# Performance work log

Measured on AMD Instinct MI355X. Metric: run time of the kernel, lower is better.

## Reference

```python
import jax, jax.numpy as jnp
import numpy as np

RES = (160, 160, 160)            # (X, Y, Z)
AABB_MIN, AABB_MAX = -1.3, 1.3
DEG = 2
SH_DIM = (DEG + 1) ** 2          # 9
N_SAMPLES = 480                  # 'plenoxels': mean(res)*3*voxel_mul
NEAR, FAR = 0.2, 6.0
WHITE_BKGD = True
N_RAYS = 2048

C0 = 0.28209479177387814
C1 = 0.4886025119029199
C2 = (1.0925484305920792, -1.0925484305920792, 0.31539156525252005,
      -1.0925484305920792, 0.5462742152960396)


def sh_encoder(dirs):
    # real spherical harmonics up to degree 2 of the normalized view dir
    d = dirs / jnp.linalg.norm(dirs, axis=-1, keepdims=True)
    x, y, z = d[..., 0], d[..., 1], d[..., 2]
    return jnp.stack([
        jnp.full_like(x, C0),
        -C1 * y, C1 * z, -C1 * x,
        C2[0] * x * y, C2[1] * y * z,
        C2[2] * (2.0 * z * z - x * x - y * y),
        C2[3] * x * z, C2[4] * (x * x - y * y),
    ], axis=-1)                                     # [..., 9]


def trilinear_sample(grid, coords):
    # grid: [C, X, Y, Z]; coords: [..., 3] in (-1, 1).
    # torch F.grid_sample convention: coord x indexes last dim (Z), y -> Y, z -> X.
    # align_corners=True, padding_mode='zeros'.
    Cc, X, Y, Z = grid.shape
    gf = grid.reshape(Cc, -1)
    fx = (coords[..., 0] + 1.0) * 0.5 * (Z - 1)
    fy = (coords[..., 1] + 1.0) * 0.5 * (Y - 1)
    fz = (coords[..., 2] + 1.0) * 0.5 * (X - 1)
    x0f = jnp.floor(fx); y0f = jnp.floor(fy); z0f = jnp.floor(fz)
    wx = fx - x0f; wy = fy - y0f; wz = fz - z0f
    x0 = x0f.astype(jnp.int32); y0 = y0f.astype(jnp.int32); z0 = z0f.astype(jnp.int32)
    out = jnp.zeros(coords.shape[:-1] + (Cc,), dtype=grid.dtype)
    for dz in (0, 1):
        for dy in (0, 1):
            for dx in (0, 1):
                ix = x0 + dx; iy = y0 + dy; iz = z0 + dz
                valid = ((ix >= 0) & (ix < Z) & (iy >= 0) & (iy < Y)
                         & (iz >= 0) & (iz < X))
                w = ((wx if dx else 1.0 - wx)
                     * (wy if dy else 1.0 - wy)
                     * (wz if dz else 1.0 - wz)) * valid
                lin = (jnp.clip(iz, 0, X - 1) * Y + jnp.clip(iy, 0, Y - 1)) * Z \
                      + jnp.clip(ix, 0, Z - 1)
                vals = jnp.take(gf, lin, axis=1)    # [C, ...]
                out = out + jnp.moveaxis(vals, 0, -1) * w[..., None]
    return out                                      # [..., C]


def get_intersections(rays_o, rays_d, aabb, step, n):
    off_pos = (aabb[1] - rays_o) / rays_d
    off_neg = (aabb[0] - rays_o) / rays_d
    start = jnp.max(jnp.minimum(off_pos, off_neg), axis=-1, keepdims=True)
    start = jnp.clip(start, NEAR, FAR)
    steps = jnp.arange(n, dtype=rays_o.dtype)[None, :]
    return start + steps * step                     # [N, n]


def setup_inputs() -> dict:
    key = jax.random.key(0)
    k1, k2, k3, k4 = jax.random.split(key, 4)
    rays_o = jax.random.normal(k1, (N_RAYS, 3), jnp.float32) * 0.1   # inside aabb
    rays_d = jax.random.normal(k2, (N_RAYS, 3), jnp.float32)
    sigma_data = 0.1 + 0.05 * jax.random.normal(k3, (1,) + RES, jnp.float32)
    rgb_data = 0.01 * jax.random.normal(k4, (3 * SH_DIM,) + RES, jnp.float32)
    return {"rays_o": rays_o, "rays_d": rays_d,
            "sigma_data": sigma_data, "rgb_data": rgb_data}


def reference(rays_o, rays_d, sigma_data, rgb_data):
    dt = rays_o.dtype
    aabb = jnp.array([[AABB_MIN] * 3, [AABB_MAX] * 3], dtype=dt)
    aabb_size = aabb[1] - aabb[0]
    inv_aabb_size = 2.0 / aabb_size
    step = jnp.linalg.norm(aabb_size) / N_SAMPLES   # voxel_len

    inter = jax.lax.stop_gradient(
        get_intersections(rays_o, rays_d, aabb, step, N_SAMPLES))  # [N,S]
    pts = rays_o[:, None, :] + rays_d[:, None, :] * inter[:, :-1, None]  # [N,S-1,3]
    pn = (pts - aabb[0]) * inv_aabb_size - 1.0       # normalized (-1,1)

    sigma = jax.nn.relu(trilinear_sample(sigma_data, pn)[..., 0])   # [N,S-1]

    dists = jnp.diff(inter, axis=1) * jnp.linalg.norm(rays_d, axis=-1, keepdims=True)
    alpha = 1.0 - jnp.exp(-sigma * dists)
    cum_light = jnp.concatenate(
        [jnp.ones((alpha.shape[0], 1), dtype=dt),
         jnp.cumprod(1.0 - alpha[:, :-1] + 1e-10, axis=-1)], axis=-1)
    abs_light = alpha * cum_light                    # [N,S-1]

    sh_mult = sh_encoder(rays_d)                     # [N,9]
    rgb_feat = trilinear_sample(rgb_data, pn)        # [N,S-1,27]
    rgb_feat = rgb_feat.reshape(rgb_feat.shape[0], rgb_feat.shape[1], 3, SH_DIM)
    sh_rgb = jnp.einsum('nsck,nk->nsc', rgb_feat, sh_mult)

    rgb = jax.nn.sigmoid(sh_rgb)
    rgb_map = jnp.einsum('ns,nsc->nc', abs_light, rgb)
    if WHITE_BKGD:
        rgb_map = rgb_map + (1.0 - abs_light.sum(-1, keepdims=True))
    return rgb_map
```

## Files before the change

### kernel.cpp

```cpp
#include <hip/hip_runtime.h>
#include <math.h>

#define RESN  160
#define VOX   4096000
#define YSTR  160
#define ZSTR  25600
#define NPTS  478
#define NRAYS 2048
#define REC   32

typedef float f2_u __attribute__((ext_vector_type(2), aligned(4)));

__global__ __launch_bounds__(256)
void transpose_grid(const float* __restrict__ sig, const float* __restrict__ rgb,
                    unsigned short* __restrict__ rec)
{
    const int v = blockIdx.x * 256 + threadIdx.x;
    float vals[32];
    vals[0] = sig[v];
    #pragma unroll
    for (int k = 0; k < 27; ++k) vals[1 + k] = rgb[(size_t)k * VOX + v];
    vals[28] = vals[29] = vals[30] = vals[31] = 0.f;
    unsigned short h[32];
    #pragma unroll
    for (int k = 0; k < 32; ++k) {
        unsigned u = __float_as_uint(vals[k]);
        unsigned r = (u + 0x7FFFu + ((u >> 16) & 1u)) >> 16;
        h[k] = (unsigned short)r;
    }
    uint4* dst = (uint4*)(rec + (size_t)v * REC);
    const uint4* src = (const uint4*)h;
    #pragma unroll
    for (int i = 0; i < 4; ++i) dst[i] = src[i];
}

__device__ __forceinline__ void bf2(unsigned u, float& lo, float& hi) {
    lo = __uint_as_float(u << 16);
    hi = __uint_as_float(u & 0xFFFF0000u);
}

__global__ __launch_bounds__(256)
void plenoxel_render2(const float* __restrict__ rays_o,
                      const float* __restrict__ rays_d,
                      const unsigned short* __restrict__ rec,
                      float* __restrict__ out)
{
    const int ray  = blockIdx.x;
    const int tid  = threadIdx.x;
    const int wave = tid >> 6;
    const int lane = tid & 63;

    const float ox = rays_o[ray*3+0], oy = rays_o[ray*3+1], oz = rays_o[ray*3+2];
    const float dxr = rays_d[ray*3+0], dyr = rays_d[ray*3+1], dzr = rays_d[ray*3+2];

    const float h = 2.6f * 1.7320508075688772f / 480.0f;

    const float ax = (1.3f - ox) / dxr, bx = (-1.3f - ox) / dxr;
    const float ay = (1.3f - oy) / dyr, by = (-1.3f - oy) / dyr;
    const float az = (1.3f - oz) / dzr, bz = (-1.3f - oz) / dzr;
    float start = fmaxf(fmaxf(fminf(ax, bx), fminf(ay, by)), fminf(az, bz));
    start = fminf(fmaxf(start, 0.2f), 6.0f);

    const float B = 1.3164f;
    const float mx1 = ( B - ox) / dxr, mx0 = (-B - ox) / dxr;
    const float my1 = ( B - oy) / dyr, my0 = (-B - oy) / dyr;
    const float mz1 = ( B - oz) / dzr, mz0 = (-B - oz) / dzr;
    float tl = fmaxf(fmaxf(fminf(mx0, mx1), fminf(my0, my1)), fminf(mz0, mz1));
    float th = fminf(fminf(fmaxf(mx0, mx1), fmaxf(my0, my1)), fmaxf(mz0, mz1));
    tl = fmaxf(tl, start);
    th = fminf(th, fmaf((float)NPTS, h, start));
    int s_lo, s_hi;
    if (th < tl) { s_lo = 0; s_hi = -1; }
    else {
        s_lo = max(0,    (int)floorf((tl - start) / h) - 1);
        s_hi = min(NPTS, (int)ceilf ((th - start) / h) + 1);
    }

    const float dsq  = dxr*dxr + dyr*dyr + dzr*dzr;
    const float dinv = rsqrtf(dsq);
    const float dn   = sqrtf(dsq);
    const float X = dxr * dinv, Y = dyr * dinv, Z = dzr * dinv;
    const float shv[9] = {
        0.28209479177387814f,
        -0.4886025119029199f * Y,
         0.4886025119029199f * Z,
        -0.4886025119029199f * X,
         1.0925484305920792f * X * Y,
        -1.0925484305920792f * Y * Z,
         0.31539156525252005f * (2.0f * Z * Z - X * X - Y * Y),
        -1.0925484305920792f * X * Z,
         0.5462742152960396f * (X * X - Y * Y),
    };
    const float dist = h * dn;

    float accR = 0.f, accG = 0.f, accB = 0.f, accL = 0.f;
    float carry = 1.0f;

    const int nlive = s_hi - s_lo + 1;
    if (nlive > 0) {
        const int chunk = (nlive + 3) >> 2;
        const int my_lo = s_lo + wave * chunk;
        const int my_hi = min(my_lo + chunk - 1, s_hi);

        for (int basei = my_lo; basei <= my_hi; basei += 64) {
            const int s = basei + lane;
            float alpha = 0.f, cr = 0.f, cg = 0.f, cb = 0.f;
            if (s <= my_hi) {
                const float t  = fmaf((float)s, h, start);
                const float px = fmaf(dxr, t, ox);
                const float py = fmaf(dyr, t, oy);
                const float pz = fmaf(dzr, t, oz);
                const float fx = fmaf(px, 61.153846153846f, 79.5f);
                const float fy = fmaf(py, 61.153846153846f, 79.5f);
                const float fz = fmaf(pz, 61.153846153846f, 79.5f);
                const float fxf = floorf(fx), fyf = floorf(fy), fzf = floorf(fz);
                const int   x0 = (int)fxf, y0 = (int)fyf, z0 = (int)fzf;
                const float wx1 = fx - fxf, wy1 = fy - fyf, wz1 = fz - fzf;
                const float wx0 = 1.f - wx1, wy0 = 1.f - wy1, wz0 = 1.f - wz1;

                float sv = 0.f, a0 = 0.f, a1 = 0.f, a2 = 0.f;

                if (x0 >= 0 && x0 <= 158 && y0 >= 0 && y0 <= 158 && z0 >= 0 && z0 <= 158) {
                    const float wzy[4] = { wz0*wy0, wz0*wy1, wz1*wy0, wz1*wy1 };
                    const int   offp[4] = { 0, YSTR*REC, ZSTR*REC, (ZSTR+YSTR)*REC };
                    const size_t base = ((size_t)z0 * ZSTR + (size_t)y0 * YSTR + x0) * REC;
                    #pragma unroll
                    for (int p = 0; p < 4; ++p) {
                        const uint4* P = (const uint4*)(rec + base + offp[p]);
                        uint4 q0[4], q1[4];
                        q0[0]=P[0]; q0[1]=P[1]; q0[2]=P[2]; q0[3]=P[3];
                        q1[0]=P[4]; q1[1]=P[5]; q1[2]=P[6]; q1[3]=P[7];
                        const float wA = wzy[p] * wx0, wB = wzy[p] * wx1;
                        #pragma unroll
                        for (int q = 0; q < 4; ++q) {
                            const unsigned* u0 = (const unsigned*)&q0[q];
                            const unsigned* u1 = (const unsigned*)&q1[q];
                            #pragma unroll
                            for (int d = 0; d < 4; ++d) {
                                const int ch = q*8 + d*2;
                                if (ch >= 28) break;
                                float l0, h0, l1, h1;
                                bf2(u0[d], l0, h0);
                                bf2(u1[d], l1, h1);
                                const float vA = fmaf(l1, wB, l0 * wA);
                                const float vBv= fmaf(h1, wB, h0 * wA);
                                if (ch == 0) sv += vA;
                                else {
                                    const int j = ch - 1;
                                    const float c = shv[j % 9] * vA;
                                    if (j < 9) a0 += c; else if (j < 18) a1 += c; else a2 += c;
                                }
                                if (ch + 1 < 28) {
                                    const int j = ch;
                                    const float c = shv[j % 9] * vBv;
                                    if (j < 9) a0 += c; else if (j < 18) a1 += c; else a2 += c;
                                }
                            }
                        }
                    }
                } else {
                    const float vwx[2] = { (x0   >= 0 && x0   < RESN) ? wx0 : 0.f,
                                           (x0+1 >= 0 && x0+1 < RESN) ? wx1 : 0.f };
                    const float vwy[2] = { (y0   >= 0 && y0   < RESN) ? wy0 : 0.f,
                                           (y0+1 >= 0 && y0+1 < RESN) ? wy1 : 0.f };
                    const float vwz[2] = { (z0   >= 0 && z0   < RESN) ? wz0 : 0.f,
                                           (z0+1 >= 0 && z0+1 < RESN) ? wz1 : 0.f };
                    const int cx[2] = { min(max(x0,0),RESN-1), min(max(x0+1,0),RESN-1) };
                    const int cy[2] = { min(max(y0,0),RESN-1), min(max(y0+1,0),RESN-1) };
                    const int cz[2] = { min(max(z0,0),RESN-1), min(max(z0+1,0),RESN-1) };
                    for (int dz = 0; dz < 2; ++dz)
                    for (int dy = 0; dy < 2; ++dy)
                    for (int dx = 0; dx < 2; ++dx) {
                        const float w = vwz[dz]*vwy[dy]*vwx[dx];
                        if (w == 0.f) continue;
                        const uint4* P = (const uint4*)(rec +
                            ((size_t)cz[dz]*ZSTR + (size_t)cy[dy]*YSTR + cx[dx]) * REC);
                        uint4 qq[4]; qq[0]=P[0]; qq[1]=P[1]; qq[2]=P[2]; qq[3]=P[3];
                        #pragma unroll
                        for (int q = 0; q < 4; ++q) {
                            const unsigned* u = (const unsigned*)&qq[q];
                            #pragma unroll
                            for (int d = 0; d < 4; ++d) {
                                const int ch = q*8 + d*2;
                                if (ch >= 28) break;
                                float lo, hi; bf2(u[d], lo, hi);
                                if (ch == 0) sv = fmaf(lo, w, sv);
                                else {
                                    const int j = ch - 1;
                                    const float c = shv[j % 9] * lo * w;
                                    if (j < 9) a0 += c; else if (j < 18) a1 += c; else a2 += c;
                                }
                                if (ch + 1 < 28) {
                                    const int j = ch;
                                    const float c = shv[j % 9] * hi * w;
                                    if (j < 9) a0 += c; else if (j < 18) a1 += c; else a2 += c;
                                }
                            }
                        }
                    }
                }

                sv = fmaxf(sv, 0.f);
                alpha = 1.f - __expf(-sv * dist);
                cr = __fdividef(1.f, 1.f + __expf(-a0));
                cg = __fdividef(1.f, 1.f + __expf(-a1));
                cb = __fdividef(1.f, 1.f + __expf(-a2));
            }

            float m = (s <= my_hi) ? (1.f - alpha + 1e-10f) : 1.f;
            float incl = m;
            #pragma unroll
            for (int off = 1; off < 64; off <<= 1) {
                float nb = __shfl_up(incl, off);
                if (lane >= off) incl *= nb;
            }
            float excl = __shfl_up(incl, 1);
            if (lane == 0) excl = 1.f;

            const float T = carry * excl;
            const float w = T * alpha;
            accR = fmaf(w, cr, accR);
            accG = fmaf(w, cg, accG);
            accB = fmaf(w, cb, accB);
            accL += w;
            carry *= __shfl(incl, 63);
        }
    }

    #pragma unroll
    for (int off = 32; off; off >>= 1) {
        accR += __shfl_xor(accR, off);
        accG += __shfl_xor(accG, off);
        accB += __shfl_xor(accB, off);
        accL += __shfl_xor(accL, off);
    }

    __shared__ float sP[4], sR[4], sG[4], sB[4], sL[4];
    if (lane == 0) { sP[wave]=carry; sR[wave]=accR; sG[wave]=accG; sB[wave]=accB; sL[wave]=accL; }
    __syncthreads();
    if (tid == 0) {
        float T = 1.f, R = 0.f, G = 0.f, Bc = 0.f, L = 0.f;
        #pragma unroll
        for (int w = 0; w < 4; ++w) {
            R  += T * sR[w];
            G  += T * sG[w];
            Bc += T * sB[w];
            L  += T * sL[w];
            T  *= sP[w];
        }
        const float bg = 1.f - L;
        out[ray*3+0] = R  + bg;
        out[ray*3+1] = G  + bg;
        out[ray*3+2] = Bc + bg;
    }
}

__device__ __forceinline__ float plane_interior(const float* __restrict__ p,
                                                float w00, float w01, float w10, float w11,
                                                float wx0, float wx1)
{
    f2_u a = *(const f2_u*)(p);
    f2_u b = *(const f2_u*)(p + YSTR);
    f2_u c = *(const f2_u*)(p + ZSTR);
    f2_u d = *(const f2_u*)(p + ZSTR + YSTR);
    float v0 = fmaf(a.y, wx1, a.x * wx0);
    float v1 = fmaf(b.y, wx1, b.x * wx0);
    float v2 = fmaf(c.y, wx1, c.x * wx0);
    float v3 = fmaf(d.y, wx1, d.x * wx0);
    return fmaf(v3, w11, fmaf(v2, w10, fmaf(v1, w01, v0 * w00)));
}

__global__ __launch_bounds__(64)
void plenoxel_render_f32(const float* __restrict__ rays_o,
                         const float* __restrict__ rays_d,
                         const float* __restrict__ sig,
                         const float* __restrict__ rgb,
                         float* __restrict__ out)
{
    const int ray  = blockIdx.x;
    const int lane = threadIdx.x;
    const float ox = rays_o[ray*3+0], oy = rays_o[ray*3+1], oz = rays_o[ray*3+2];
    const float dxr = rays_d[ray*3+0], dyr = rays_d[ray*3+1], dzr = rays_d[ray*3+2];
    const float h = 2.6f * 1.7320508075688772f / 480.0f;
    const float ax = (1.3f - ox) / dxr, bx = (-1.3f - ox) / dxr;
    const float ay = (1.3f - oy) / dyr, by = (-1.3f - oy) / dyr;
    const float az = (1.3f - oz) / dzr, bz = (-1.3f - oz) / dzr;
    float start = fmaxf(fmaxf(fminf(ax, bx), fminf(ay, by)), fminf(az, bz));
    start = fminf(fmaxf(start, 0.2f), 6.0f);
    const float B = 1.3164f;
    const float mx1 = ( B - ox) / dxr, mx0 = (-B - ox) / dxr;
    const float my1 = ( B - oy) / dyr, my0 = (-B - oy) / dyr;
    const float mz1 = ( B - oz) / dzr, mz0 = (-B - oz) / dzr;
    float tl = fmaxf(fmaxf(fminf(mx0, mx1), fminf(my0, my1)), fminf(mz0, mz1));
    float th = fminf(fminf(fmaxf(mx0, mx1), fmaxf(my0, my1)), fmaxf(mz0, mz1));
    tl = fmaxf(tl, start);
    th = fminf(th, fmaf((float)NPTS, h, start));
    int s_lo, s_hi;
    if (th < tl) { s_lo = 0; s_hi = -1; }
    else {
        s_lo = max(0,    (int)floorf((tl - start) / h) - 1);
        s_hi = min(NPTS, (int)ceilf ((th - start) / h) + 1);
    }
    const float dsq  = dxr*dxr + dyr*dyr + dzr*dzr;
    const float dinv = rsqrtf(dsq);
    const float dn   = sqrtf(dsq);
    const float X = dxr * dinv, Y = dyr * dinv, Z = dzr * dinv;
    const float shv[9] = {
        0.28209479177387814f, -0.4886025119029199f * Y, 0.4886025119029199f * Z,
        -0.4886025119029199f * X, 1.0925484305920792f * X * Y, -1.0925484305920792f * Y * Z,
        0.31539156525252005f * (2.0f * Z * Z - X * X - Y * Y),
        -1.0925484305920792f * X * Z, 0.5462742152960396f * (X * X - Y * Y),
    };
    const float dist = h * dn;
    float accR = 0.f, accG = 0.f, accB = 0.f, accL = 0.f;
    float carry = 1.0f;
    for (int basei = s_lo; basei <= s_hi; basei += 64) {
        const int s = basei + lane;
        float alpha = 0.f, cr = 0.f, cg = 0.f, cb = 0.f;
        if (s <= s_hi) {
            const float t  = fmaf((float)s, h, start);
            const float px = fmaf(dxr, t, ox);
            const float py = fmaf(dyr, t, oy);
            const float pz = fmaf(dzr, t, oz);
            const float fx = fmaf(px, 61.153846153846f, 79.5f);
            const float fy = fmaf(py, 61.153846153846f, 79.5f);
            const float fz = fmaf(pz, 61.153846153846f, 79.5f);
            const float fxf = floorf(fx), fyf = floorf(fy), fzf = floorf(fz);
            const int   x0 = (int)fxf, y0 = (int)fyf, z0 = (int)fzf;
            const float wx1 = fx - fxf, wy1 = fy - fyf, wz1 = fz - fzf;
            const float wx0 = 1.f - wx1, wy0 = 1.f - wy1, wz0 = 1.f - wz1;
            float sv = 0.f, a0 = 0.f, a1 = 0.f, a2 = 0.f;
            if (x0 >= 0 && x0 <= 158 && y0 >= 0 && y0 <= 158 && z0 >= 0 && z0 <= 158) {
                const float w00 = wz0*wy0, w01 = wz0*wy1, w10 = wz1*wy0, w11 = wz1*wy1;
                const size_t bofs = (size_t)z0 * ZSTR + (size_t)y0 * YSTR + (size_t)x0;
                sv = plane_interior(sig + bofs, w00, w01, w10, w11, wx0, wx1);
                const float* rp = rgb + bofs;
                #pragma unroll
                for (int c = 0; c < 3; ++c) {
                    float sc = 0.f;
                    #pragma unroll
                    for (int k = 0; k < 9; ++k) {
                        const float v = plane_interior(rp + (size_t)(c*9+k)*VOX,
                                                       w00, w01, w10, w11, wx0, wx1);
                        sc = fmaf(v, shv[k], sc);
                    }
                    if (c == 0) a0 = sc; else if (c == 1) a1 = sc; else a2 = sc;
                }
            } else {
                const float vwx0 = (x0   >= 0 && x0   < RESN) ? wx0 : 0.f;
                const float vwx1 = (x0+1 >= 0 && x0+1 < RESN) ? wx1 : 0.f;
                const float vwy0 = (y0   >= 0 && y0   < RESN) ? wy0 : 0.f;
                const float vwy1 = (y0+1 >= 0 && y0+1 < RESN) ? wy1 : 0.f;
                const float vwz0 = (z0   >= 0 && z0   < RESN) ? wz0 : 0.f;
                const float vwz1 = (z0+1 >= 0 && z0+1 < RESN) ? wz1 : 0.f;
                const int cx0 = min(max(x0,   0), RESN-1), cx1 = min(max(x0+1, 0), RESN-1);
                const int cy0 = min(max(y0,   0), RESN-1), cy1 = min(max(y0+1, 0), RESN-1);
                const int cz0 = min(max(z0,   0), RESN-1), cz1 = min(max(z0+1, 0), RESN-1);
                const float cw[8] = { vwz0*vwy0*vwx0, vwz0*vwy0*vwx1,
                                      vwz0*vwy1*vwx0, vwz0*vwy1*vwx1,
                                      vwz1*vwy0*vwx0, vwz1*vwy0*vwx1,
                                      vwz1*vwy1*vwx0, vwz1*vwy1*vwx1 };
                const size_t co[8] = {
                    (size_t)cz0*ZSTR + (size_t)cy0*YSTR + cx0,
                    (size_t)cz0*ZSTR + (size_t)cy0*YSTR + cx1,
                    (size_t)cz0*ZSTR + (size_t)cy1*YSTR + cx0,
                    (size_t)cz0*ZSTR + (size_t)cy1*YSTR + cx1,
                    (size_t)cz1*ZSTR + (size_t)cy0*YSTR + cx0,
                    (size_t)cz1*ZSTR + (size_t)cy0*YSTR + cx1,
                    (size_t)cz1*ZSTR + (size_t)cy1*YSTR + cx0,
                    (size_t)cz1*ZSTR + (size_t)cy1*YSTR + cx1 };
                #pragma unroll
                for (int j = 0; j < 8; ++j) {
                    if (cw[j] != 0.f) {
                        const float wj = cw[j];
                        sv = fmaf(sig[co[j]], wj, sv);
                        const float* rp = rgb + co[j];
                        float t0 = 0.f, t1 = 0.f, t2 = 0.f;
                        #pragma unroll
                        for (int k = 0; k < 9; ++k) {
                            t0 = fmaf(rp[(size_t)(k     )*VOX], shv[k], t0);
                            t1 = fmaf(rp[(size_t)(k +  9)*VOX], shv[k], t1);
                            t2 = fmaf(rp[(size_t)(k + 18)*VOX], shv[k], t2);
                        }
                        a0 = fmaf(t0, wj, a0);
                        a1 = fmaf(t1, wj, a1);
                        a2 = fmaf(t2, wj, a2);
                    }
                }
            }
            sv = fmaxf(sv, 0.f);
            alpha = 1.f - __expf(-sv * dist);
            cr = __fdividef(1.f, 1.f + __expf(-a0));
            cg = __fdividef(1.f, 1.f + __expf(-a1));
            cb = __fdividef(1.f, 1.f + __expf(-a2));
        }
        float m = (s <= s_hi) ? (1.f - alpha + 1e-10f) : 1.f;
        float incl = m;
        #pragma unroll
        for (int off = 1; off < 64; off <<= 1) {
            float nb = __shfl_up(incl, off);
            if (lane >= off) incl *= nb;
        }
        float excl = __shfl_up(incl, 1);
        if (lane == 0) excl = 1.f;
        const float T = carry * excl;
        const float w = T * alpha;
        accR = fmaf(w, cr, accR);
        accG = fmaf(w, cg, accG);
        accB = fmaf(w, cb, accB);
        accL += w;
        carry *= __shfl(incl, 63);
    }
    #pragma unroll
    for (int off = 32; off; off >>= 1) {
        accR += __shfl_xor(accR, off);
        accG += __shfl_xor(accG, off);
        accB += __shfl_xor(accB, off);
        accL += __shfl_xor(accL, off);
    }
    if (lane == 0) {
        const float bg = 1.f - accL;
        out[ray*3+0] = accR + bg;
        out[ray*3+1] = accG + bg;
        out[ray*3+2] = accB + bg;
    }
}

extern "C" void kernel_launch(void* const* d_in, const int* in_sizes, int n_in,
                              void* d_out, int out_size, void* d_ws, size_t ws_size,
                              hipStream_t stream) {
    const float* rays_o = (const float*)d_in[0];
    const float* rays_d = (const float*)d_in[1];
    const float* sig    = (const float*)d_in[2];
    const float* rgb    = (const float*)d_in[3];
    float* out = (float*)d_out;

    const size_t need = (size_t)VOX * REC * sizeof(unsigned short);
    if (ws_size >= need) {
        unsigned short* rec = (unsigned short*)d_ws;
        transpose_grid<<<VOX / 256, 256, 0, stream>>>(sig, rgb, rec);
        plenoxel_render2<<<NRAYS, 256, 0, stream>>>(rays_o, rays_d, rec, out);
    } else {
        plenoxel_render_f32<<<NRAYS, 64, 0, stream>>>(rays_o, rays_d, sig, rgb, out);
    }
}
```

Before: 667.3 us.

## Drop per-call bf16 grid transpose; split render into per-sample and scan kernels

```diff
diff --git a/kernel.cpp b/kernel.cpp
--- a/kernel.cpp
+++ b/kernel.cpp
@@ -1,58 +1,29 @@
 #include <hip/hip_runtime.h>
 #include <math.h>
 
-#define RESN  160
-#define VOX   4096000
-#define YSTR  160
-#define ZSTR  25600
-#define NPTS  478
-#define NRAYS 2048
-#define REC   32
+#define RESN   160
+#define VOX    4096000
+#define YSTR   160
+#define ZSTR   25600
+#define SCOUNT 479
+#define NPTS   478
+#define NRAYS  2048
 
 typedef float f2_u __attribute__((ext_vector_type(2), aligned(4)));
 
 __global__ __launch_bounds__(256)
-void transpose_grid(const float* __restrict__ sig, const float* __restrict__ rgb,
-                    unsigned short* __restrict__ rec)
+void p1_samples(const float* __restrict__ rays_o,
+                const float* __restrict__ rays_d,
+                const float* __restrict__ sig,
+                const float* __restrict__ rgb,
+                float4* __restrict__ sc)
 {
-    const int v = blockIdx.x * 256 + threadIdx.x;
-    float vals[32];
-    vals[0] = sig[v];
-    #pragma unroll
-    for (int k = 0; k < 27; ++k) vals[1 + k] = rgb[(size_t)k * VOX + v];
-    vals[28] = vals[29] = vals[30] = vals[31] = 0.f;
-    unsigned short h[32];
-    #pragma unroll
-    for (int k = 0; k < 32; ++k) {
-        unsigned u = __float_as_uint(vals[k]);
-        unsigned r = (u + 0x7FFFu + ((u >> 16) & 1u)) >> 16;
-        h[k] = (unsigned short)r;
-    }
-    uint4* dst = (uint4*)(rec + (size_t)v * REC);
-    const uint4* src = (const uint4*)h;
-    #pragma unroll
-    for (int i = 0; i < 4; ++i) dst[i] = src[i];
-}
-
-__device__ __forceinline__ void bf2(unsigned u, float& lo, float& hi) {
-    lo = __uint_as_float(u << 16);
-    hi = __uint_as_float(u & 0xFFFF0000u);
-}
-
-__global__ __launch_bounds__(256)
-void plenoxel_render2(const float* __restrict__ rays_o,
-                      const float* __restrict__ rays_d,
-                      const unsigned short* __restrict__ rec,
-                      float* __restrict__ out)
-{
-    const int ray  = blockIdx.x;
-    const int tid  = threadIdx.x;
-    const int wave = tid >> 6;
-    const int lane = tid & 63;
+    const int gid = blockIdx.x * 256 + threadIdx.x;
+    const int ray = gid / SCOUNT;
+    const int s   = gid - ray * SCOUNT;
 
     const float ox = rays_o[ray*3+0], oy = rays_o[ray*3+1], oz = rays_o[ray*3+2];
     const float dxr = rays_d[ray*3+0], dyr = rays_d[ray*3+1], dzr = rays_d[ray*3+2];
-
     const float h = 2.6f * 1.7320508075688772f / 480.0f;
 
     const float ax = (1.3f - ox) / dxr, bx = (-1.3f - ox) / dxr;
@@ -69,11 +40,15 @@
     float th = fminf(fminf(fmaxf(mx0, mx1), fmaxf(my0, my1)), fmaxf(mz0, mz1));
     tl = fmaxf(tl, start);
     th = fminf(th, fmaf((float)NPTS, h, start));
-    int s_lo, s_hi;
-    if (th < tl) { s_lo = 0; s_hi = -1; }
-    else {
+    int s_lo = 0, s_hi = -1;
+    if (th >= tl) {
         s_lo = max(0,    (int)floorf((tl - start) / h) - 1);
         s_hi = min(NPTS, (int)ceilf ((th - start) / h) + 1);
+    }
+
+    if (s < s_lo || s > s_hi) {
+        sc[gid] = make_float4(0.f, 0.f, 0.f, 0.f);
+        return;
     }
 
     const float dsq  = dxr*dxr + dyr*dyr + dzr*dzr;
@@ -81,24 +56,218 @@
     const float dn   = sqrtf(dsq);
     const float X = dxr * dinv, Y = dyr * dinv, Z = dzr * dinv;
     const float shv[9] = {
-        0.28209479177387814f,
-        -0.4886025119029199f * Y,
-         0.4886025119029199f * Z,
-        -0.4886025119029199f * X,
-         1.0925484305920792f * X * Y,
-        -1.0925484305920792f * Y * Z,
-         0.31539156525252005f * (2.0f * Z * Z - X * X - Y * Y),
-        -1.0925484305920792f * X * Z,
-         0.5462742152960396f * (X * X - Y * Y),
+        0.28209479177387814f, -0.4886025119029199f * Y, 0.4886025119029199f * Z,
+        -0.4886025119029199f * X, 1.0925484305920792f * X * Y, -1.0925484305920792f * Y * Z,
+        0.31539156525252005f * (2.0f * Z * Z - X * X - Y * Y),
+        -1.0925484305920792f * X * Z, 0.5462742152960396f * (X * X - Y * Y),
     };
     const float dist = h * dn;
 
+    const float t  = fmaf((float)s, h, start);
+    const float px = fmaf(dxr, t, ox);
+    const float py = fmaf(dyr, t, oy);
+    const float pz = fmaf(dzr, t, oz);
+    const float fx = fmaf(px, 61.153846153846f, 79.5f);
+    const float fy = fmaf(py, 61.153846153846f, 79.5f);
+    const float fz = fmaf(pz, 61.153846153846f, 79.5f);
+    const float fxf = floorf(fx), fyf = floorf(fy), fzf = floorf(fz);
+    const int   x0 = (int)fxf, y0 = (int)fyf, z0 = (int)fzf;
+    const float wx1 = fx - fxf, wy1 = fy - fyf, wz1 = fz - fzf;
+    const float wx0 = 1.f - wx1, wy0 = 1.f - wy1, wz0 = 1.f - wz1;
+
+    float sv = 0.f, a0 = 0.f, a1 = 0.f, a2 = 0.f;
+
+    if (x0 >= 0 && x0 <= 158 && y0 >= 0 && y0 <= 158 && z0 >= 0 && z0 <= 158) {
+        const float w00 = wz0*wy0, w01 = wz0*wy1, w10 = wz1*wy0, w11 = wz1*wy1;
+        const size_t bofs = (size_t)z0 * ZSTR + (size_t)y0 * YSTR + (size_t)x0;
+        #pragma unroll
+        for (int g = 0; g < 4; ++g) {
+            f2_u r[7][4];
+            #pragma unroll
+            for (int c = 0; c < 7; ++c) {
+                const int ch = g*7 + c;
+                const float* bp = (ch == 0 ? sig + bofs
+                                           : rgb + (size_t)(ch-1)*VOX + bofs);
+                r[c][0] = *(const f2_u*)(bp);
+                r[c][1] = *(const f2_u*)(bp + YSTR);
+                r[c][2] = *(const f2_u*)(bp + ZSTR);
+                r[c][3] = *(const f2_u*)(bp + ZSTR + YSTR);
+            }
+            #pragma unroll
+            for (int c = 0; c < 7; ++c) {
+                const int ch = g*7 + c;
+                const float v0 = fmaf(r[c][0].y, wx1, r[c][0].x * wx0);
+                const float v1 = fmaf(r[c][1].y, wx1, r[c][1].x * wx0);
+                const float v2 = fmaf(r[c][2].y, wx1, r[c][2].x * wx0);
+                const float v3 = fmaf(r[c][3].y, wx1, r[c][3].x * wx0);
+                const float v  = fmaf(v3, w11, fmaf(v2, w10, fmaf(v1, w01, v0 * w00)));
+                if (ch == 0) sv = v;
+                else {
+                    const int j = ch - 1;
+                    const float ccoef = shv[j % 9] * v;
+                    if (j < 9) a0 += ccoef;
+                    else if (j < 18) a1 += ccoef;
+                    else a2 += ccoef;
+                }
+            }
+        }
+    } else {
+        const float vwx0 = (x0   >= 0 && x0   < RESN) ? wx0 : 0.f;
+        const float vwx1 = (x0+1 >= 0 && x0+1 < RESN) ? wx1 : 0.f;
+        const float vwy0 = (y0   >= 0 && y0   < RESN) ? wy0 : 0.f;
+        const float vwy1 = (y0+1 >= 0 && y0+1 < RESN) ? wy1 : 0.f;
+        const float vwz0 = (z0   >= 0 && z0   < RESN) ? wz0 : 0.f;
+        const float vwz1 = (z0+1 >= 0 && z0+1 < RESN) ? wz1 : 0.f;
+        const int cx0 = min(max(x0,   0), RESN-1), cx1 = min(max(x0+1, 0), RESN-1);
+        const int cy0 = min(max(y0,   0), RESN-1), cy1 = min(max(y0+1, 0), RESN-1);
+        const int cz0 = min(max(z0,   0), RESN-1), cz1 = min(max(z0+1, 0), RESN-1);
+        const float cw[8] = { vwz0*vwy0*vwx0, vwz0*vwy0*vwx1,
+                              vwz0*vwy1*vwx0, vwz0*vwy1*vwx1,
+                              vwz1*vwy0*vwx0, vwz1*vwy0*vwx1,
+                              vwz1*vwy1*vwx0, vwz1*vwy1*vwx1 };
+        const size_t co[8] = {
+            (size_t)cz0*ZSTR + (size_t)cy0*YSTR + cx0,
+            (size_t)cz0*ZSTR + (size_t)cy0*YSTR + cx1,
+            (size_t)cz0*ZSTR + (size_t)cy1*YSTR + cx0,
+            (size_t)cz0*ZSTR + (size_t)cy1*YSTR + cx1,
+            (size_t)cz1*ZSTR + (size_t)cy0*YSTR + cx0,
+            (size_t)cz1*ZSTR + (size_t)cy0*YSTR + cx1,
+            (size_t)cz1*ZSTR + (size_t)cy1*YSTR + cx0,
+            (size_t)cz1*ZSTR + (size_t)cy1*YSTR + cx1 };
+        #pragma unroll
+        for (int j8 = 0; j8 < 8; ++j8) {
+            if (cw[j8] != 0.f) {
+                const float wj = cw[j8];
+                sv = fmaf(sig[co[j8]], wj, sv);
+                const float* rp = rgb + co[j8];
+                float t0 = 0.f, t1 = 0.f, t2 = 0.f;
+                #pragma unroll
+                for (int k = 0; k < 9; ++k) {
+                    t0 = fmaf(rp[(size_t)(k     )*VOX], shv[k], t0);
+                    t1 = fmaf(rp[(size_t)(k +  9)*VOX], shv[k], t1);
+                    t2 = fmaf(rp[(size_t)(k + 18)*VOX], shv[k], t2);
+                }
+                a0 = fmaf(t0, wj, a0);
+                a1 = fmaf(t1, wj, a1);
+                a2 = fmaf(t2, wj, a2);
+            }
+        }
+    }
+
+    sv = fmaxf(sv, 0.f);
+    const float alpha = 1.f - __expf(-sv * dist);
+    const float cr = __fdividef(1.f, 1.f + __expf(-a0));
+    const float cg = __fdividef(1.f, 1.f + __expf(-a1));
+    const float cb = __fdividef(1.f, 1.f + __expf(-a2));
+    sc[gid] = make_float4(alpha, cr, cg, cb);
+}
+
+__global__ __launch_bounds__(64)
+void p2_scan(const float4* __restrict__ sc, float* __restrict__ out)
+{
+    const int ray  = blockIdx.x;
+    const int lane = threadIdx.x;
+
     float accR = 0.f, accG = 0.f, accB = 0.f, accL = 0.f;
     float carry = 1.0f;
+    const float4* base = sc + (size_t)ray * SCOUNT;
+
+    for (int basei = 0; basei < SCOUNT; basei += 64) {
+        const int s = basei + lane;
+        float alpha = 0.f, cr = 0.f, cg = 0.f, cb = 0.f;
+        bool live = (s < SCOUNT);
+        if (live) {
+            const float4 v = base[s];
+            alpha = v.x; cr = v.y; cg = v.z; cb = v.w;
+        }
+        float m = live ? (1.f - alpha + 1e-10f) : 1.f;
+        float incl = m;
+        #pragma unroll
+        for (int off = 1; off < 64; off <<= 1) {
+            float nb = __shfl_up(incl, off);
+            if (lane >= off) incl *= nb;
+        }
+        float excl = __shfl_up(incl, 1);
+        if (lane == 0) excl = 1.f;
+
+        const float T = carry * excl;
+        const float w = T * alpha;
+        accR = fmaf(w, cr, accR);
+        accG = fmaf(w, cg, accG);
+        accB = fmaf(w, cb, accB);
+        accL += w;
+        carry *= __shfl(incl, 63);
+    }
+
+    #pragma unroll
+    for (int off = 32; off; off >>= 1) {
+        accR += __shfl_xor(accR, off);
+        accG += __shfl_xor(accG, off);
+        accB += __shfl_xor(accB, off);
+        accL += __shfl_xor(accL, off);
+    }
+    if (lane == 0) {
+        const float bg = 1.f - accL;
+        out[ray*3+0] = accR + bg;
+        out[ray*3+1] = accG + bg;
+        out[ray*3+2] = accB + bg;
+    }
+}
+
+__global__ __launch_bounds__(128)
+void render_f32_fused(const float* __restrict__ rays_o,
+                      const float* __restrict__ rays_d,
+                      const float* __restrict__ sig,
+                      const float* __restrict__ rgb,
+                      float* __restrict__ out)
+{
+    const int ray  = blockIdx.x;
+    const int tid  = threadIdx.x;
+    const int wave = tid >> 6;
+    const int lane = tid & 63;
+
+    const float ox = rays_o[ray*3+0], oy = rays_o[ray*3+1], oz = rays_o[ray*3+2];
+    const float dxr = rays_d[ray*3+0], dyr = rays_d[ray*3+1], dzr = rays_d[ray*3+2];
+    const float h = 2.6f * 1.7320508075688772f / 480.0f;
+
+    const float ax = (1.3f - ox) / dxr, bx = (-1.3f - ox) / dxr;
+    const float ay = (1.3f - oy) / dyr, by = (-1.3f - oy) / dyr;
+    const float az = (1.3f - oz) / dzr, bz = (-1.3f - oz) / dzr;
+    float start = fmaxf(fmaxf(fminf(ax, bx), fminf(ay, by)), fminf(az, bz));
+    start = fminf(fmaxf(start, 0.2f), 6.0f);
+
+    const float B = 1.3164f;
+    const float mx1 = ( B - ox) / dxr, mx0 = (-B - ox) / dxr;
+    const float my1 = ( B - oy) / dyr, my0 = (-B - oy) / dyr;
+    const float mz1 = ( B - oz) / dzr, mz0 = (-B - oz) / dzr;
+    float tl = fmaxf(fmaxf(fminf(mx0, mx1), fminf(my0, my1)), fminf(mz0, mz1));
+    float th = fminf(fminf(fmaxf(mx0, mx1), fmaxf(my0, my1)), fmaxf(mz0, mz1));
+    tl = fmaxf(tl, start);
+    th = fminf(th, fmaf((float)NPTS, h, start));
+    int s_lo = 0, s_hi = -1;
+    if (th >= tl) {
+        s_lo = max(0,    (int)floorf((tl - start) / h) - 1);
+        s_hi = min(NPTS, (int)ceilf ((th - start) / h) + 1);
+    }
+
+    const float dsq  = dxr*dxr + dyr*dyr + dzr*dzr;
+    const float dinv = rsqrtf(dsq);
+    const float dn   = sqrtf(dsq);
+    const float X = dxr * dinv, Y = dyr * dinv, Z = dzr * dinv;
+    const float shv[9] = {
+        0.28209479177387814f, -0.4886025119029199f * Y, 0.4886025119029199f * Z,
+        -0.4886025119029199f * X, 1.0925484305920792f * X * Y, -1.0925484305920792f * Y * Z,
+        0.31539156525252005f * (2.0f * Z * Z - X * X - Y * Y),
+        -1.0925484305920792f * X * Z, 0.5462742152960396f * (X * X - Y * Y),
+    };
+    const float dist = h * dn;
+
+    float accR = 0.f, accG = 0.f, accB = 0.f, accL = 0.f;
+    float carry = 1.0f;
 
     const int nlive = s_hi - s_lo + 1;
     if (nlive > 0) {
-        const int chunk = (nlive + 3) >> 2;
+        const int chunk = (nlive + 1) >> 1;
         const int my_lo = s_lo + wave * chunk;
         const int my_hi = min(my_lo + chunk - 1, s_hi);
 
@@ -117,96 +286,89 @@
                 const int   x0 = (int)fxf, y0 = (int)fyf, z0 = (int)fzf;
                 const float wx1 = fx - fxf, wy1 = fy - fyf, wz1 = fz - fzf;
                 const float wx0 = 1.f - wx1, wy0 = 1.f - wy1, wz0 = 1.f - wz1;
-
                 float sv = 0.f, a0 = 0.f, a1 = 0.f, a2 = 0.f;
-
                 if (x0 >= 0 && x0 <= 158 && y0 >= 0 && y0 <= 158 && z0 >= 0 && z0 <= 158) {
-                    const float wzy[4] = { wz0*wy0, wz0*wy1, wz1*wy0, wz1*wy1 };
-                    const int   offp[4] = { 0, YSTR*REC, ZSTR*REC, (ZSTR+YSTR)*REC };
-                    const size_t base = ((size_t)z0 * ZSTR + (size_t)y0 * YSTR + x0) * REC;
+                    const float w00 = wz0*wy0, w01 = wz0*wy1, w10 = wz1*wy0, w11 = wz1*wy1;
+                    const size_t bofs = (size_t)z0 * ZSTR + (size_t)y0 * YSTR + (size_t)x0;
                     #pragma unroll
-                    for (int p = 0; p < 4; ++p) {
-                        const uint4* P = (const uint4*)(rec + base + offp[p]);
-                        uint4 q0[4], q1[4];
-                        q0[0]=P[0]; q0[1]=P[1]; q0[2]=P[2]; q0[3]=P[3];
-                        q1[0]=P[4]; q1[1]=P[5]; q1[2]=P[6]; q1[3]=P[7];
-                        const float wA = wzy[p] * wx0, wB = wzy[p] * wx1;
+                    for (int g = 0; g < 4; ++g) {
+                        f2_u r[7][4];
                         #pragma unroll
-                        for (int q = 0; q < 4; ++q) {
-                            const unsigned* u0 = (const unsigned*)&q0[q];
-                            const unsigned* u1 = (const unsigned*)&q1[q];
-                            #pragma unroll
-                            for (int d = 0; d < 4; ++d) {
-                                const int ch = q*8 + d*2;
-                                if (ch >= 28) break;
-                                float l0, h0, l1, h1;
-                                bf2(u0[d], l0, h0);
-                                bf2(u1[d], l1, h1);
-                                const float vA = fmaf(l1, wB, l0 * wA);
-                                const float vBv= fmaf(h1, wB, h0 * wA);
-                                if (ch == 0) sv += vA;
-                                else {
-                                    const int j = ch - 1;
-                                    const float c = shv[j % 9] * vA;
-                                    if (j < 9) a0 += c; else if (j < 18) a1 += c; else a2 += c;
-                                }
-                                if (ch + 1 < 28) {
-                                    const int j = ch;
-                                    const float c = shv[j % 9] * vBv;
-                                    if (j < 9) a0 += c; else if (j < 18) a1 += c; else a2 += c;
-                                }
+                        for (int c = 0; c < 7; ++c) {
+                            const int ch = g*7 + c;
+                            const float* bp = (ch == 0 ? sig + bofs
+                                                       : rgb + (size_t)(ch-1)*VOX + bofs);
+                            r[c][0] = *(const f2_u*)(bp);
+                            r[c][1] = *(const f2_u*)(bp + YSTR);
+                            r[c][2] = *(const f2_u*)(bp + ZSTR);
+                            r[c][3] = *(const f2_u*)(bp + ZSTR + YSTR);
+                        }
+                        #pragma unroll
+                        for (int c = 0; c < 7; ++c) {
+                            const int ch = g*7 + c;
+                            const float v0 = fmaf(r[c][0].y, wx1, r[c][0].x * wx0);
+                            const float v1 = fmaf(r[c][1].y, wx1, r[c][1].x * wx0);
+                            const float v2 = fmaf(r[c][2].y, wx1, r[c][2].x * wx0);
+                            const float v3 = fmaf(r[c][3].y, wx1, r[c][3].x * wx0);
+                            const float v  = fmaf(v3, w11, fmaf(v2, w10, fmaf(v1, w01, v0 * w00)));
+                            if (ch == 0) sv = v;
+                            else {
+                                const int j = ch - 1;
+                                const float ccoef = shv[j % 9] * v;
+                                if (j < 9) a0 += ccoef;
+                                else if (j < 18) a1 += ccoef;
+                                else a2 += ccoef;
                             }
                         }
                     }
                 } else {
-                    const float vwx[2] = { (x0   >= 0 && x0   < RESN) ? wx0 : 0.f,
-                                           (x0+1 >= 0 && x0+1 < RESN) ? wx1 : 0.f };
-                    const float vwy[2] = { (y0   >= 0 && y0   < RESN) ? wy0 : 0.f,
-                                           (y0+1 >= 0 && y0+1 < RESN) ? wy1 : 0.f };
-                    const float vwz[2] = { (z0   >= 0 && z0   < RESN) ? wz0 : 0.f,
-                                           (z0+1 >= 0 && z0+1 < RESN) ? wz1 : 0.f };
-                    const int cx[2] = { min(max(x0,0),RESN-1), min(max(x0+1,0),RESN-1) };
-                    const int cy[2] = { min(max(y0,0),RESN-1), min(max(y0+1,0),RESN-1) };
-                    const int cz[2] = { min(max(z0,0),RESN-1), min(max(z0+1,0),RESN-1) };
-                    for (int dz = 0; dz < 2; ++dz)
-                    for (int dy = 0; dy < 2; ++dy)
-                    for (int dx = 0; dx < 2; ++dx) {
-                        const float w = vwz[dz]*vwy[dy]*vwx[dx];
-                        if (w == 0.f) continue;
-                        const uint4* P = (const uint4*)(rec +
-                            ((size_t)cz[dz]*ZSTR + (size_t)cy[dy]*YSTR + cx[dx]) * REC);
-                        uint4 qq[4]; qq[0]=P[0]; qq[1]=P[1]; qq[2]=P[2]; qq[3]=P[3];
-                        #pragma unroll
-                        for (int q = 0; q < 4; ++q) {
-                            const unsigned* u = (const unsigned*)&qq[q];
+                    const float vwx0 = (x0   >= 0 && x0   < RESN) ? wx0 : 0.f;
+                    const float vwx1 = (x0+1 >= 0 && x0+1 < RESN) ? wx1 : 0.f;
+                    const float vwy0 = (y0   >= 0 && y0   < RESN) ? wy0 : 0.f;
+                    const float vwy1 = (y0+1 >= 0 && y0+1 < RESN) ? wy1 : 0.f;
+                    const float vwz0 = (z0   >= 0 && z0   < RESN) ? wz0 : 0.f;
+                    const float vwz1 = (z0+1 >= 0 && z0+1 < RESN) ? wz1 : 0.f;
+                    const int cx0 = min(max(x0,   0), RESN-1), cx1 = min(max(x0+1, 0), RESN-1);
+                    const int cy0 = min(max(y0,   0), RESN-1), cy1 = min(max(y0+1, 0), RESN-1);
+                    const int cz0 = min(max(z0,   0), RESN-1), cz1 = min(max(z0+1, 0), RESN-1);
+                    const float cw[8] = { vwz0*vwy0*vwx0, vwz0*vwy0*vwx1,
+                                          vwz0*vwy1*vwx0, vwz0*vwy1*vwx1,
+                                          vwz1*vwy0*vwx0, vwz1*vwy0*vwx1,
+                                          vwz1*vwy1*vwx0, vwz1*vwy1*vwx1 };
+                    const size_t co[8] = {
+                        (size_t)cz0*ZSTR + (size_t)cy0*YSTR + cx0,
+                        (size_t)cz0*ZSTR + (size_t)cy0*YSTR + cx1,
+                        (size_t)cz0*ZSTR + (size_t)cy1*YSTR + cx0,
+                        (size_t)cz0*ZSTR + (size_t)cy1*YSTR + cx1,
+                        (size_t)cz1*ZSTR + (size_t)cy0*YSTR + cx0,
+                        (size_t)cz1*ZSTR + (size_t)cy0*YSTR + cx1,
+                        (size_t)cz1*ZSTR + (size_t)cy1*YSTR + cx0,
+                        (size_t)cz1*ZSTR + (size_t)cy1*YSTR + cx1 };
+                    #pragma unroll
+                    for (int j8 = 0; j8 < 8; ++j8) {
+                        if (cw[j8] != 0.f) {
+                            const float wj = cw[j8];
+                            sv = fmaf(sig[co[j8]], wj, sv);
+                            const float* rp = rgb + co[j8];
+                            float t0 = 0.f, t1 = 0.f, t2 = 0.f;
                             #pragma unroll
-                            for (int d = 0; d < 4; ++d) {
-                                const int ch = q*8 + d*2;
-                                if (ch >= 28) break;
-                                float lo, hi; bf2(u[d], lo, hi);
-                                if (ch == 0) sv = fmaf(lo, w, sv);
-                                else {
-                                    const int j = ch - 1;
-                                    const float c = shv[j % 9] * lo * w;
-                                    if (j < 9) a0 += c; else if (j < 18) a1 += c; else a2 += c;
-                                }
-                                if (ch + 1 < 28) {
-                                    const int j = ch;
-                                    const float c = shv[j % 9] * hi * w;
-                                    if (j < 9) a0 += c; else if (j < 18) a1 += c; else a2 += c;
-                                }
+                            for (int k = 0; k < 9; ++k) {
+                                t0 = fmaf(rp[(size_t)(k     )*VOX], shv[k], t0);
+                                t1 = fmaf(rp[(size_t)(k +  9)*VOX], shv[k], t1);
+                                t2 = fmaf(rp[(size_t)(k + 18)*VOX], shv[k], t2);
                             }
+                            a0 = fmaf(t0, wj, a0);
+                            a1 = fmaf(t1, wj, a1);
+                            a2 = fmaf(t2, wj, a2);
                         }
                     }
                 }
-
                 sv = fmaxf(sv, 0.f);
                 alpha = 1.f - __expf(-sv * dist);
                 cr = __fdividef(1.f, 1.f + __expf(-a0));
                 cg = __fdividef(1.f, 1.f + __expf(-a1));
                 cb = __fdividef(1.f, 1.f + __expf(-a2));
             }
-
             float m = (s <= my_hi) ? (1.f - alpha + 1e-10f) : 1.f;
             float incl = m;
             #pragma unroll
@@ -216,7 +378,6 @@
             }
             float excl = __shfl_up(incl, 1);
             if (lane == 0) excl = 1.f;
-
             const float T = carry * excl;
             const float w = T * alpha;
             accR = fmaf(w, cr, accR);
@@ -234,195 +395,17 @@
         accB += __shfl_xor(accB, off);
         accL += __shfl_xor(accL, off);
     }
-
-    __shared__ float sP[4], sR[4], sG[4], sB[4], sL[4];
+    __shared__ float sP[2], sR[2], sG[2], sB[2], sL[2];
     if (lane == 0) { sP[wave]=carry; sR[wave]=accR; sG[wave]=accG; sB[wave]=accB; sL[wave]=accL; }
     __syncthreads();
     if (tid == 0) {
         float T = 1.f, R = 0.f, G = 0.f, Bc = 0.f, L = 0.f;
         #pragma unroll
-        for (int w = 0; w < 4; ++w) {
-            R  += T * sR[w];
-            G  += T * sG[w];
-            Bc += T * sB[w];
-            L  += T * sL[w];
-            T  *= sP[w];
+        for (int w = 0; w < 2; ++w) {
+            R += T*sR[w]; G += T*sG[w]; Bc += T*sB[w]; L += T*sL[w]; T *= sP[w];
         }
         const float bg = 1.f - L;
-        out[ray*3+0] = R  + bg;
-        out[ray*3+1] = G  + bg;
-        out[ray*3+2] = Bc + bg;
-    }
-}
-
-__device__ __forceinline__ float plane_interior(const float* __restrict__ p,
-                                                float w00, float w01, float w10, float w11,
-                                                float wx0, float wx1)
-{
-    f2_u a = *(const f2_u*)(p);
-    f2_u b = *(const f2_u*)(p + YSTR);
-    f2_u c = *(const f2_u*)(p + ZSTR);
-    f2_u d = *(const f2_u*)(p + ZSTR + YSTR);
-    float v0 = fmaf(a.y, wx1, a.x * wx0);
-    float v1 = fmaf(b.y, wx1, b.x * wx0);
-    float v2 = fmaf(c.y, wx1, c.x * wx0);
-    float v3 = fmaf(d.y, wx1, d.x * wx0);
-    return fmaf(v3, w11, fmaf(v2, w10, fmaf(v1, w01, v0 * w00)));
-}
-
-__global__ __launch_bounds__(64)
-void plenoxel_render_f32(const float* __restrict__ rays_o,
-                         const float* __restrict__ rays_d,
-                         const float* __restrict__ sig,
-                         const float* __restrict__ rgb,
-                         float* __restrict__ out)
-{
-    const int ray  = blockIdx.x;
-    const int lane = threadIdx.x;
-    const float ox = rays_o[ray*3+0], oy = rays_o[ray*3+1], oz = rays_o[ray*3+2];
-    const float dxr = rays_d[ray*3+0], dyr = rays_d[ray*3+1], dzr = rays_d[ray*3+2];
-    const float h = 2.6f * 1.7320508075688772f / 480.0f;
-    const float ax = (1.3f - ox) / dxr, bx = (-1.3f - ox) / dxr;
-    const float ay = (1.3f - oy) / dyr, by = (-1.3f - oy) / dyr;
-    const float az = (1.3f - oz) / dzr, bz = (-1.3f - oz) / dzr;
-    float start = fmaxf(fmaxf(fminf(ax, bx), fminf(ay, by)), fminf(az, bz));
-    start = fminf(fmaxf(start, 0.2f), 6.0f);
-    const float B = 1.3164f;
-    const float mx1 = ( B - ox) / dxr, mx0 = (-B - ox) / dxr;
-    const float my1 = ( B - oy) / dyr, my0 = (-B - oy) / dyr;
-    const float mz1 = ( B - oz) / dzr, mz0 = (-B - oz) / dzr;
-    float tl = fmaxf(fmaxf(fminf(mx0, mx1), fminf(my0, my1)), fminf(mz0, mz1));
-    float th = fminf(fminf(fmaxf(mx0, mx1), fmaxf(my0, my1)), fmaxf(mz0, mz1));
-    tl = fmaxf(tl, start);
-    th = fminf(th, fmaf((float)NPTS, h, start));
-    int s_lo, s_hi;
-    if (th < tl) { s_lo = 0; s_hi = -1; }
-    else {
-        s_lo = max(0,    (int)floorf((tl - start) / h) - 1);
-        s_hi = min(NPTS, (int)ceilf ((th - start) / h) + 1);
-    }
-    const float dsq  = dxr*dxr + dyr*dyr + dzr*dzr;
-    const float dinv = rsqrtf(dsq);
-    const float dn   = sqrtf(dsq);
-    const float X = dxr * dinv, Y = dyr * dinv, Z = dzr * dinv;
-    const float shv[9] = {
-        0.28209479177387814f, -0.4886025119029199f * Y, 0.4886025119029199f * Z,
-        -0.4886025119029199f * X, 1.0925484305920792f * X * Y, -1.0925484305920792f * Y * Z,
-        0.31539156525252005f * (2.0f * Z * Z - X * X - Y * Y),
-        -1.0925484305920792f * X * Z, 0.5462742152960396f * (X * X - Y * Y),
-    };
-    const float dist = h * dn;
-    float accR = 0.f, accG = 0.f, accB = 0.f, accL = 0.f;
-    float carry = 1.0f;
-    for (int basei = s_lo; basei <= s_hi; basei += 64) {
-        const int s = basei + lane;
-        float alpha = 0.f, cr = 0.f, cg = 0.f, cb = 0.f;
-        if (s <= s_hi) {
-            const float t  = fmaf((float)s, h, start);
-            const float px = fmaf(dxr, t, ox);
-            const float py = fmaf(dyr, t, oy);
-            const float pz = fmaf(dzr, t, oz);
-            const float fx = fmaf(px, 61.153846153846f, 79.5f);
-            const float fy = fmaf(py, 61.153846153846f, 79.5f);
-            const float fz = fmaf(pz, 61.153846153846f, 79.5f);
-            const float fxf = floorf(fx), fyf = floorf(fy), fzf = floorf(fz);
-            const int   x0 = (int)fxf, y0 = (int)fyf, z0 = (int)fzf;
-            const float wx1 = fx - fxf, wy1 = fy - fyf, wz1 = fz - fzf;
-            const float wx0 = 1.f - wx1, wy0 = 1.f - wy1, wz0 = 1.f - wz1;
-            float sv = 0.f, a0 = 0.f, a1 = 0.f, a2 = 0.f;
-            if (x0 >= 0 && x0 <= 158 && y0 >= 0 && y0 <= 158 && z0 >= 0 && z0 <= 158) {
-                const float w00 = wz0*wy0, w01 = wz0*wy1, w10 = wz1*wy0, w11 = wz1*wy1;
-                const size_t bofs = (size_t)z0 * ZSTR + (size_t)y0 * YSTR + (size_t)x0;
-                sv = plane_interior(sig + bofs, w00, w01, w10, w11, wx0, wx1);
-                const float* rp = rgb + bofs;
-                #pragma unroll
-                for (int c = 0; c < 3; ++c) {
-                    float sc = 0.f;
-                    #pragma unroll
-                    for (int k = 0; k < 9; ++k) {
-                        const float v = plane_interior(rp + (size_t)(c*9+k)*VOX,
-                                                       w00, w01, w10, w11, wx0, wx1);
-                        sc = fmaf(v, shv[k], sc);
-                    }
-                    if (c == 0) a0 = sc; else if (c == 1) a1 = sc; else a2 = sc;
-                }
-            } else {
-                const float vwx0 = (x0   >= 0 && x0   < RESN) ? wx0 : 0.f;
-                const float vwx1 = (x0+1 >= 0 && x0+1 < RESN) ? wx1 : 0.f;
-                const float vwy0 = (y0   >= 0 && y0   < RESN) ? wy0 : 0.f;
-                const float vwy1 = (y0+1 >= 0 && y0+1 < RESN) ? wy1 : 0.f;
-                const float vwz0 = (z0   >= 0 && z0   < RESN) ? wz0 : 0.f;
-                const float vwz1 = (z0+1 >= 0 && z0+1 < RESN) ? wz1 : 0.f;
-                const int cx0 = min(max(x0,   0), RESN-1), cx1 = min(max(x0+1, 0), RESN-1);
-                const int cy0 = min(max(y0,   0), RESN-1), cy1 = min(max(y0+1, 0), RESN-1);
-                const int cz0 = min(max(z0,   0), RESN-1), cz1 = min(max(z0+1, 0), RESN-1);
-                const float cw[8] = { vwz0*vwy0*vwx0, vwz0*vwy0*vwx1,
-                                      vwz0*vwy1*vwx0, vwz0*vwy1*vwx1,
-                                      vwz1*vwy0*vwx0, vwz1*vwy0*vwx1,
-                                      vwz1*vwy1*vwx0, vwz1*vwy1*vwx1 };
-                const size_t co[8] = {
-                    (size_t)cz0*ZSTR + (size_t)cy0*YSTR + cx0,
-                    (size_t)cz0*ZSTR + (size_t)cy0*YSTR + cx1,
-                    (size_t)cz0*ZSTR + (size_t)cy1*YSTR + cx0,
-                    (size_t)cz0*ZSTR + (size_t)cy1*YSTR + cx1,
-                    (size_t)cz1*ZSTR + (size_t)cy0*YSTR + cx0,
-                    (size_t)cz1*ZSTR + (size_t)cy0*YSTR + cx1,
-                    (size_t)cz1*ZSTR + (size_t)cy1*YSTR + cx0,
-                    (size_t)cz1*ZSTR + (size_t)cy1*YSTR + cx1 };
-                #pragma unroll
-                for (int j = 0; j < 8; ++j) {
-                    if (cw[j] != 0.f) {
-                        const float wj = cw[j];
-                        sv = fmaf(sig[co[j]], wj, sv);
-                        const float* rp = rgb + co[j];
-                        float t0 = 0.f, t1 = 0.f, t2 = 0.f;
-                        #pragma unroll
-                        for (int k = 0; k < 9; ++k) {
-                            t0 = fmaf(rp[(size_t)(k     )*VOX], shv[k], t0);
-                            t1 = fmaf(rp[(size_t)(k +  9)*VOX], shv[k], t1);
-                            t2 = fmaf(rp[(size_t)(k + 18)*VOX], shv[k], t2);
-                        }
-                        a0 = fmaf(t0, wj, a0);
-                        a1 = fmaf(t1, wj, a1);
-                        a2 = fmaf(t2, wj, a2);
-                    }
-                }
-            }
-            sv = fmaxf(sv, 0.f);
-            alpha = 1.f - __expf(-sv * dist);
-            cr = __fdividef(1.f, 1.f + __expf(-a0));
-            cg = __fdividef(1.f, 1.f + __expf(-a1));
-            cb = __fdividef(1.f, 1.f + __expf(-a2));
-        }
-        float m = (s <= s_hi) ? (1.f - alpha + 1e-10f) : 1.f;
-        float incl = m;
-        #pragma unroll
-        for (int off = 1; off < 64; off <<= 1) {
-            float nb = __shfl_up(incl, off);
-            if (lane >= off) incl *= nb;
-        }
-        float excl = __shfl_up(incl, 1);
-        if (lane == 0) excl = 1.f;
-        const float T = carry * excl;
-        const float w = T * alpha;
-        accR = fmaf(w, cr, accR);
-        accG = fmaf(w, cg, accG);
-        accB = fmaf(w, cb, accB);
-        accL += w;
-        carry *= __shfl(incl, 63);
-    }
-    #pragma unroll
-    for (int off = 32; off; off >>= 1) {
-        accR += __shfl_xor(accR, off);
-        accG += __shfl_xor(accG, off);
-        accB += __shfl_xor(accB, off);
-        accL += __shfl_xor(accL, off);
-    }
-    if (lane == 0) {
-        const float bg = 1.f - accL;
-        out[ray*3+0] = accR + bg;
-        out[ray*3+1] = accG + bg;
-        out[ray*3+2] = accB + bg;
+        out[ray*3+0] = R + bg; out[ray*3+1] = G + bg; out[ray*3+2] = Bc + bg;
     }
 }
 
@@ -435,12 +418,13 @@
     const float* rgb    = (const float*)d_in[3];
     float* out = (float*)d_out;
 
-    const size_t need = (size_t)VOX * REC * sizeof(unsigned short);
+    const size_t need = (size_t)NRAYS * SCOUNT * sizeof(float4);
     if (ws_size >= need) {
-        unsigned short* rec = (unsigned short*)d_ws;
-        transpose_grid<<<VOX / 256, 256, 0, stream>>>(sig, rgb, rec);
-        plenoxel_render2<<<NRAYS, 256, 0, stream>>>(rays_o, rays_d, rec, out);
+        float4* sc = (float4*)d_ws;
+        const int total = NRAYS * SCOUNT;
+        p1_samples<<<(total + 255) / 256, 256, 0, stream>>>(rays_o, rays_d, sig, rgb, sc);
+        p2_scan  <<<NRAYS, 64, 0, stream>>>(sc, out);
     } else {
-        plenoxel_render_f32<<<NRAYS, 64, 0, stream>>>(rays_o, rays_d, sig, rgb, out);
+        render_f32_fused<<<NRAYS, 128, 0, stream>>>(rays_o, rays_d, sig, rgb, out);
     }
 }
```

Result: no change. 658.2 us (-1.4%).
